# Performance work log

Hardware: AMD Instinct MI355X
Metric: run time of the kernel (lower is better)

Reference implementation:

```python
import jax, jax.numpy as jnp
import numpy as np

N, M, E = 400000, 100000, 3200000
C_FEAT = 61            # per-point feature channels
D_IN = 64              # 3 (rel xyz) + C_FEAT
D0, D1, D2 = 64, 128, 256  # mlp = [64, 128, 256]
EPS = 1e-5


def setup_inputs() -> dict:
    key = jax.random.key(0)
    ks = jax.random.split(key, 16)
    inp = {}
    inp['point_bxyz'] = jax.random.uniform(ks[0], (N, 4), dtype=jnp.float32) * 50.0
    inp['point_feat'] = jax.random.normal(ks[1], (N, C_FEAT), dtype=jnp.float32)
    inp['sample_idx'] = jax.random.randint(ks[2], (M,), 0, N)
    inp['e_point'] = jax.random.randint(ks[3], (E,), 0, N)
    inp['e_new'] = jnp.sort(jax.random.randint(ks[4], (E,), 0, M))
    # PointConv: Linear(D_IN -> D0)
    inp['W0'] = jax.random.normal(ks[5], (D_IN, D0), dtype=jnp.float32) / np.sqrt(D_IN)
    inp['b0'] = jnp.zeros((D0,), dtype=jnp.float32)
    # mlp_convs[0]: Linear(D0 -> D1) + BN
    inp['W1'] = jax.random.normal(ks[6], (D0, D1), dtype=jnp.float32) / np.sqrt(D0)
    inp['b1'] = jnp.zeros((D1,), dtype=jnp.float32)
    inp['g1'] = jnp.ones((D1,), dtype=jnp.float32)
    inp['beta1'] = jnp.zeros((D1,), dtype=jnp.float32)
    # mlp_convs[1]: Linear(D1 -> D2) + BN
    inp['W2'] = jax.random.normal(ks[7], (D1, D2), dtype=jnp.float32) / np.sqrt(D1)
    inp['b2'] = jnp.zeros((D2,), dtype=jnp.float32)
    inp['g2'] = jnp.ones((D2,), dtype=jnp.float32)
    inp['beta2'] = jnp.zeros((D2,), dtype=jnp.float32)
    return inp


def _bn_relu(x, g, b):
    # BatchNorm1d in training mode: batch stats, biased variance
    mu = x.mean(axis=0)
    var = x.var(axis=0)
    return jax.nn.relu((x - mu) * jax.lax.rsqrt(var + EPS) * g + b)


def reference(point_bxyz, point_feat, sample_idx, e_point, e_new,
              W0, b0, W1, b1, g1, beta1, W2, b2, g2, beta2):
    num_new = sample_idx.shape[0]
    new_bxyz = point_bxyz[sample_idx]                      # [M, 4]
    # PointConv: per-edge relative position encoding + feature gather
    rel = point_bxyz[e_point, 1:4] - new_bxyz[e_new, 1:4]  # [E, 3]
    edge_in = jnp.concatenate([rel, point_feat[e_point]], axis=-1)  # [E, D_IN]
    h = jax.nn.relu(edge_in @ W0 + b0)                     # [E, D0]
    # per-neighborhood max aggregation (scatter-max), empty segments -> 0
    agg = jax.ops.segment_max(h, e_new, num_segments=num_new)
    agg = jnp.where(jnp.isneginf(agg), 0.0, agg)           # [M, D0]
    # trailing Linear + BN + ReLU stack
    x = _bn_relu(agg @ W1 + b1, g1, beta1)                 # [M, D1]
    x = _bn_relu(x @ W2 + b2, g2, beta2)                   # [M, D2]
    return new_bxyz, x
```

## Files before the change

kernel.cpp:

```cpp
#include <hip/hip_runtime.h>

#define EPS 1e-5f
#define ECHUNK 64

typedef _Float16 half8 __attribute__((ext_vector_type(8)));
typedef _Float16 half4v __attribute__((ext_vector_type(4)));
typedef float float4v __attribute__((ext_vector_type(4)));

static __device__ __forceinline__ unsigned pkmax16(unsigned a, unsigned b) {
    unsigned d;
    asm("v_pk_max_f16 %0, %1, %2" : "=v"(d) : "v"(a), "v"(b));
    return d;
}

__global__ void gather_kernel(const float4* __restrict__ bxyz, const int* __restrict__ sidx,
                              float4* __restrict__ out, int M) {
    int i = blockIdx.x * blockDim.x + threadIdx.x;
    if (i < M) out[i] = bxyz[sidx[i]];
}

__global__ void prep_kernel(const float* __restrict__ W0, const float* __restrict__ W1,
                            const float* __restrict__ W2, _Float16* __restrict__ W0t,
                            _Float16* __restrict__ W1t, _Float16* __restrict__ W2t) {
    int i = blockIdx.x * blockDim.x + threadIdx.x;
    if (i < 4096) {
        int k = i >> 6, n = i & 63;
        W0t[(size_t)n * 64 + k] = (_Float16)W0[i];
    } else if (i < 12288) {
        int j = i - 4096; int k = j >> 7, n = j & 127;
        W1t[(size_t)n * 64 + k] = (_Float16)W1[j];
    } else if (i < 45056) {
        int j = i - 12288; int k = j >> 8, n = j & 255;
        W2t[(size_t)n * 128 + k] = (_Float16)W2[j];
    }
}

__global__ __launch_bounds__(256, 4) void point_kernel(
    const float* __restrict__ feat, const float4* __restrict__ bxyz4,
    const _Float16* __restrict__ W0t, const float* __restrict__ b0,
    _Float16* __restrict__ GDh, int N) {
    __shared__ _Float16 As[128 * 72];
    int t = threadIdx.x;
    int row0 = blockIdx.x * 128;
    if (t < 128) {
        int r = min(row0 + t, N - 1);
        float4 P = bxyz4[r];
        As[t * 72 + 0] = (_Float16)P.y;
        As[t * 72 + 1] = (_Float16)P.z;
        As[t * 72 + 2] = (_Float16)P.w;
    }
    const float* fbase = feat + (size_t)row0 * 61;
    int avail = (int)min((size_t)7808, (size_t)(N - row0) * 61);
#pragma unroll
    for (int j = 0; j < 8; ++j) {
        int base = (t + j * 256) * 4;
        if (base < avail) {
            float4 v = *(const float4*)&fbase[base];
            float fv[4] = {v.x, v.y, v.z, v.w};
#pragma unroll
            for (int u = 0; u < 4; ++u) {
                int flat = base + u;
                int r = flat / 61;
                int k = flat - r * 61;
                As[r * 72 + 3 + k] = (_Float16)fv[u];
            }
        }
    }
    __syncthreads();
    int w = t >> 6, lane = t & 63, quad = lane >> 4, l16 = lane & 15;
    int mwave = w * 32;
    float4v acc[2][4] = {};
#pragma unroll
    for (int kc = 0; kc < 2; ++kc) {
        int koff = kc * 32 + quad * 8;
        half8 af[2], bf[4];
#pragma unroll
        for (int mt = 0; mt < 2; ++mt)
            af[mt] = *(const half8*)&As[(mwave + mt * 16 + l16) * 72 + koff];
#pragma unroll
        for (int nt = 0; nt < 4; ++nt)
            bf[nt] = *(const half8*)&W0t[(size_t)(nt * 16 + l16) * 64 + koff];
#pragma unroll
        for (int mt = 0; mt < 2; ++mt)
#pragma unroll
            for (int nt = 0; nt < 4; ++nt)
                acc[mt][nt] = __builtin_amdgcn_mfma_f32_16x16x32_f16(af[mt], bf[nt], acc[mt][nt], 0, 0, 0);
    }
    float b0v[4];
#pragma unroll
    for (int nt = 0; nt < 4; ++nt) b0v[nt] = b0[nt * 16 + l16];
    __syncthreads();
#pragma unroll
    for (int mt = 0; mt < 2; ++mt)
#pragma unroll
        for (int i = 0; i < 4; ++i) {
            int rloc = mwave + mt * 16 + quad * 4 + i;
#pragma unroll
            for (int nt = 0; nt < 4; ++nt)
                As[rloc * 72 + nt * 16 + l16] = (_Float16)(acc[mt][nt][i] + b0v[nt]);
        }
    __syncthreads();
#pragma unroll
    for (int j = 0; j < 4; ++j) {
        int i8 = t + j * 256;
        int r = i8 >> 3, c8 = i8 & 7;
        if (row0 + r < N)
            *(half8*)&GDh[(size_t)(row0 + r) * 64 + c8 * 8] = *(const half8*)&As[r * 72 + c8 * 8];
    }
}

__global__ __launch_bounds__(256, 8) void edge_kernel(
    const float4* __restrict__ nbxyz4,
    const int* __restrict__ e_point, const int* __restrict__ e_new,
    const _Float16* __restrict__ GDh, const float* __restrict__ W0,
    float* __restrict__ agg, int E) {
    int lane = threadIdx.x & 63;
    int gwave = blockIdx.x * 4 + (threadIdx.x >> 6);
    int base = __builtin_amdgcn_readfirstlane(gwave * ECHUNK);
    if (base >= E) return;
    int n = min(ECHUNK, E - base);

    if (n == ECHUNK) {
        bool hi = lane >= 32;
        int c0 = lane & 31;
        int ch = c0 * 2 + (hi ? 1 : 0);
        float wx = W0[ch], wy = W0[64 + ch], wz = W0[128 + ch];
        const unsigned NEGP = 0xFBFFFBFFu;

        int ep = e_point[base + lane];
        int en = e_new[base + lane];

        int prev = __shfl_up(en, 1);
        unsigned long long bm = __ballot(lane == 0 || en != prev);
        unsigned blo = __builtin_amdgcn_readfirstlane((unsigned)bm);
        unsigned bhi = __builtin_amdgcn_readfirstlane((unsigned)(bm >> 32));
        unsigned long long bmask = (((unsigned long long)bhi << 32) | blo) & ~1ull;

        int curseg = __builtin_amdgcn_readlane(en, 0);
        unsigned amax = NEGP;
        int laneoff = c0 * 4;
        int permbase = hi ? 4 : 0;

#define FLUSH_SEG()  do {                                                          \
        unsigned other_ = (unsigned)__shfl_xor((int)amax, 32);                     \
        unsigned comb_ = pkmax16(amax, other_);                                    \
        unsigned bits_ = hi ? (comb_ >> 16) : (comb_ & 0xffffu);                   \
        _Float16 hm_ = __builtin_bit_cast(_Float16, (unsigned short)bits_);        \
        float4 Q_ = nbxyz4[curseg];                                                \
        float S_ = fmaf(Q_.y, wx, fmaf(Q_.z, wy, Q_.w * wz));                      \
        float v_ = fmaxf(0.f, (float)hm_ - S_);                                    \
        atomicMax((int*)&agg[(size_t)curseg * 64 + ch], __float_as_int(v_));       \
    } while (0)

#pragma unroll
        for (int grp = 0; grp < 2; ++grp) {
            unsigned gu[16];
#pragma unroll
            for (int j = 0; j < 16; ++j) {
                int p = __builtin_amdgcn_ds_bpermute(permbase + (grp * 16 + j) * 8, ep);
                unsigned off = ((unsigned)p << 7) + laneoff;
                gu[j] = *(const unsigned*)((const char*)GDh + off);
            }
#pragma unroll
            for (int j = 0; j < 16; ++j) {
                int e0 = (grp * 16 + j) * 2;
                if ((bmask >> e0) & 1) {
                    FLUSH_SEG();
                    curseg = __builtin_amdgcn_readlane(en, e0);
                    amax = NEGP;
                }
                if ((bmask >> (e0 + 1)) & 1) {
                    amax = pkmax16(amax, hi ? NEGP : gu[j]);
                    FLUSH_SEG();
                    curseg = __builtin_amdgcn_readlane(en, e0 + 1);
                    amax = hi ? gu[j] : NEGP;
                } else {
                    amax = pkmax16(amax, gu[j]);
                }
            }
        }
        FLUSH_SEG();
#undef FLUSH_SEG
    } else {
        float wx = W0[lane], wy = W0[64 + lane], wz = W0[128 + lane];
        int idx = min(base + lane, E - 1);
        int ep = e_point[idx];
        int en = e_new[idx];
        int curseg = -1;
        float runmax = 0.f, S = 0.f;
        for (int e = 0; e < n; ++e) {
            int p = __builtin_amdgcn_readlane(ep, e);
            int s = __builtin_amdgcn_readlane(en, e);
            if (s != curseg) {
                if (curseg >= 0)
                    atomicMax((int*)&agg[(size_t)curseg * 64 + lane], __float_as_int(runmax));
                curseg = s;
                runmax = 0.f;
                float4 Q = nbxyz4[s];
                S = fmaf(Q.y, wx, fmaf(Q.z, wy, Q.w * wz));
            }
            float h = (float)GDh[(size_t)p * 64 + lane] - S;
            runmax = fmaxf(runmax, h);
        }
        if (curseg >= 0)
            atomicMax((int*)&agg[(size_t)curseg * 64 + lane], __float_as_int(runmax));
    }
}

__global__ __launch_bounds__(256, 2) void gemm1_kernel(
    const float* __restrict__ agg, const _Float16* __restrict__ W1t,
    _Float16* __restrict__ y1h, float* __restrict__ p1sum, float* __restrict__ p1sq, int M) {
    __shared__ _Float16 As[128 * 72];
    __shared__ float red[4096];
    int t = threadIdx.x;
    int row0 = blockIdx.x * 128;
#pragma unroll
    for (int j = 0; j < 8; ++j) {
        int i4 = t + j * 256;
        int r = i4 >> 4, k4 = i4 & 15;
        float4 v = make_float4(0.f, 0.f, 0.f, 0.f);
        if (row0 + r < M) v = ((const float4*)agg)[(size_t)(row0 + r) * 16 + k4];
        half4v h;
        h[0] = (_Float16)v.x; h[1] = (_Float16)v.y; h[2] = (_Float16)v.z; h[3] = (_Float16)v.w;
        *(half4v*)&As[r * 72 + k4 * 4] = h;
    }
    __syncthreads();
    int w = t >> 6, lane = t & 63, quad = lane >> 4, l16 = lane & 15;
    int mwave = w * 32;
    float4v acc[2][8] = {};
#pragma unroll
    for (int kc = 0; kc < 2; ++kc) {
        int koff = kc * 32 + quad * 8;
        half8 af[2], bf[8];
#pragma unroll
        for (int mt = 0; mt < 2; ++mt)
            af[mt] = *(const half8*)&As[(mwave + mt * 16 + l16) * 72 + koff];
#pragma unroll
        for (int nt = 0; nt < 8; ++nt)
            bf[nt] = *(const half8*)&W1t[(size_t)(nt * 16 + l16) * 64 + koff];
#pragma unroll
        for (int mt = 0; mt < 2; ++mt)
#pragma unroll
            for (int nt = 0; nt < 8; ++nt)
                acc[mt][nt] = __builtin_amdgcn_mfma_f32_16x16x32_f16(af[mt], bf[nt], acc[mt][nt], 0, 0, 0);
    }
    float s[8] = {}, q[8] = {};
#pragma unroll
    for (int mt = 0; mt < 2; ++mt)
#pragma unroll
        for (int i = 0; i < 4; ++i)
#pragma unroll
            for (int nt = 0; nt < 8; ++nt) {
                float a = acc[mt][nt][i];
                s[nt] += a; q[nt] += a * a;
            }
    int slot = w * 4 + quad;
#pragma unroll
    for (int nt = 0; nt < 8; ++nt) {
        int c = nt * 16 + l16;
        red[c * 16 + slot] = s[nt];
        red[2048 + c * 16 + slot] = q[nt];
    }
    __syncthreads();
    if (t < 128) {
        float ss = 0.f, qq = 0.f;
#pragma unroll
        for (int i = 0; i < 16; ++i) { ss += red[t * 16 + i]; qq += red[2048 + t * 16 + i]; }
        p1sum[(size_t)blockIdx.x * 128 + t] = ss;
        p1sq[(size_t)blockIdx.x * 128 + t] = qq;
    }
#pragma unroll
    for (int half = 0; half < 2; ++half) {
#pragma unroll
        for (int mt = 0; mt < 2; ++mt)
#pragma unroll
            for (int i = 0; i < 4; ++i) {
                int rloc = mwave + mt * 16 + quad * 4 + i;
#pragma unroll
                for (int nt = 0; nt < 4; ++nt)
                    As[rloc * 72 + nt * 16 + l16] = (_Float16)acc[mt][half * 4 + nt][i];
            }
        __syncthreads();
#pragma unroll
        for (int j = 0; j < 4; ++j) {
            int i8 = t + j * 256;
            int r = i8 >> 3, c8 = i8 & 7;
            if (row0 + r < M)
                *(half8*)&y1h[(size_t)(row0 + r) * 128 + half * 64 + c8 * 8] =
                    *(const half8*)&As[r * 72 + c8 * 8];
        }
        __syncthreads();
    }
}

__global__ void stats_kernel(const float* __restrict__ psum, const float* __restrict__ psq,
                             const float* __restrict__ g, const float* __restrict__ beta,
                             float* __restrict__ scale, float* __restrict__ shift,
                             int nblk, int ncols, float invM) {
    __shared__ float ss[256], qq[256];
    int c = blockIdx.x;
    int t = threadIdx.x;
    float s = 0.f, q = 0.f;
    for (int b = t; b < nblk; b += 256) {
        s += psum[(size_t)b * ncols + c];
        q += psq[(size_t)b * ncols + c];
    }
    ss[t] = s; qq[t] = q;
    __syncthreads();
    for (int off = 128; off > 0; off >>= 1) {
        if (t < off) { ss[t] += ss[t + off]; qq[t] += qq[t + off]; }
        __syncthreads();
    }
    if (t == 0) {
        float mean = ss[0] * invM;
        float var = qq[0] * invM - mean * mean;
        float sc = g[c] * rsqrtf(var + EPS);
        scale[c] = sc;
        shift[c] = beta[c] - mean * sc;
    }
}

__global__ __launch_bounds__(256, 2) void gemm2_kernel(
    const _Float16* __restrict__ y1h, const _Float16* __restrict__ W2t,
    const float* __restrict__ scale1, const float* __restrict__ shift1,
    float* __restrict__ yout, float* __restrict__ p2sum, float* __restrict__ p2sq,
    int M, int nbn) {
    __shared__ _Float16 As[128 * 136];
    __shared__ _Float16 Bs[128 * 136];
    int t = threadIdx.x;
    int bm = blockIdx.x / nbn;
    int bn = blockIdx.x % nbn;
    int row0 = bm * 128;
#pragma unroll
    for (int j = 0; j < 8; ++j) {
        int i8 = t + j * 256;
        int r = i8 >> 4, k8 = i8 & 15;
        half8 hv = {};
        if (row0 + r < M) {
            half8 y = *(const half8*)&y1h[(size_t)(row0 + r) * 128 + k8 * 8];
            float4 sca = ((const float4*)scale1)[k8 * 2];
            float4 scb = ((const float4*)scale1)[k8 * 2 + 1];
            float4 sha = ((const float4*)shift1)[k8 * 2];
            float4 shb = ((const float4*)shift1)[k8 * 2 + 1];
            float sc[8] = {sca.x, sca.y, sca.z, sca.w, scb.x, scb.y, scb.z, scb.w};
            float sh[8] = {sha.x, sha.y, sha.z, sha.w, shb.x, shb.y, shb.z, shb.w};
#pragma unroll
            for (int u = 0; u < 8; ++u)
                hv[u] = (_Float16)fmaxf(0.f, fmaf((float)y[u], sc[u], sh[u]));
        }
        *(half8*)&As[r * 136 + k8 * 8] = hv;
    }
    int n0 = bn * 128;
#pragma unroll
    for (int j = 0; j < 8; ++j) {
        int i8 = t + j * 256;
        int nn = i8 >> 4, k8 = i8 & 15;
        *(half8*)&Bs[nn * 136 + k8 * 8] = *(const half8*)&W2t[(size_t)(n0 + nn) * 128 + k8 * 8];
    }
    __syncthreads();
    int w = t >> 6, lane = t & 63;
    int quad = lane >> 4, l16 = lane & 15;
    int mwave = (w >> 1) * 64, nwave = (w & 1) * 64;
    float4v acc[4][4] = {};
#pragma unroll
    for (int kc = 0; kc < 4; ++kc) {
        int koff = kc * 32 + quad * 8;
        half8 af[4], bf[4];
#pragma unroll
        for (int mt = 0; mt < 4; ++mt)
            af[mt] = *(const half8*)&As[(mwave + mt * 16 + l16) * 136 + koff];
#pragma unroll
        for (int nt = 0; nt < 4; ++nt)
            bf[nt] = *(const half8*)&Bs[(nwave + nt * 16 + l16) * 136 + koff];
#pragma unroll
        for (int mt = 0; mt < 4; ++mt)
#pragma unroll
            for (int nt = 0; nt < 4; ++nt)
                acc[mt][nt] = __builtin_amdgcn_mfma_f32_16x16x32_f16(af[mt], bf[nt], acc[mt][nt], 0, 0, 0);
    }
    float s[4] = {}, q[4] = {};
    int colbase = n0 + nwave + l16;
#pragma unroll
    for (int mt = 0; mt < 4; ++mt) {
#pragma unroll
        for (int i = 0; i < 4; ++i) {
            int row = row0 + mwave + mt * 16 + quad * 4 + i;
            if (row < M) {
#pragma unroll
                for (int nt = 0; nt < 4; ++nt)
                    yout[(size_t)row * 256 + colbase + nt * 16] = acc[mt][nt][i];
            }
#pragma unroll
            for (int nt = 0; nt < 4; ++nt) {
                float a = acc[mt][nt][i];
                s[nt] += a; q[nt] += a * a;
            }
        }
    }
    __syncthreads();
    float* red = (float*)As;
    int slot = (w >> 1) * 4 + quad;
#pragma unroll
    for (int nt = 0; nt < 4; ++nt) {
        int c = (w & 1) * 64 + nt * 16 + l16;
        red[c * 8 + slot] = s[nt];
        red[1024 + c * 8 + slot] = q[nt];
    }
    __syncthreads();
    if (t < 128) {
        float ss = 0.f, qq = 0.f;
#pragma unroll
        for (int i = 0; i < 8; ++i) { ss += red[t * 8 + i]; qq += red[1024 + t * 8 + i]; }
        p2sum[(size_t)bm * 256 + n0 + t] = ss;
        p2sq[(size_t)bm * 256 + n0 + t] = qq;
    }
}

__global__ void apply2_kernel(float4* __restrict__ x, const float* __restrict__ scale2,
                              const float* __restrict__ shift2, int n4) {
    int i = blockIdx.x * blockDim.x + threadIdx.x;
    if (i >= n4) return;
    int c4 = i & 63;
    float4 v = x[i];
    float4 sc = ((const float4*)scale2)[c4];
    float4 sh = ((const float4*)shift2)[c4];
    v.x = fmaxf(0.f, fmaf(v.x, sc.x, sh.x));
    v.y = fmaxf(0.f, fmaf(v.y, sc.y, sh.y));
    v.z = fmaxf(0.f, fmaf(v.z, sc.z, sh.z));
    v.w = fmaxf(0.f, fmaf(v.w, sc.w, sh.w));
    x[i] = v;
}

extern "C" void kernel_launch(void* const* d_in, const int* in_sizes, int n_in,
                              void* d_out, int out_size, void* d_ws, size_t ws_size,
                              hipStream_t stream) {
    const float* bxyz  = (const float*)d_in[0];
    const float* feat  = (const float*)d_in[1];
    const int*   sidx  = (const int*)d_in[2];
    const int*   e_point = (const int*)d_in[3];
    const int*   e_new = (const int*)d_in[4];
    const float* W0    = (const float*)d_in[5];
    const float* b0    = (const float*)d_in[6];
    const float* W1    = (const float*)d_in[7];
    const float* g1    = (const float*)d_in[9];
    const float* beta1 = (const float*)d_in[10];
    const float* W2    = (const float*)d_in[11];
    const float* g2    = (const float*)d_in[13];
    const float* beta2 = (const float*)d_in[14];
    int N = in_sizes[0] / 4;
    int M = in_sizes[2];
    int E = in_sizes[3];

    float* out0 = (float*)d_out;
    float* out1 = (float*)d_out + (size_t)M * 4;

    float* ws = (float*)d_ws;
    size_t o = 0;
    float* agg = ws + o; o += (size_t)M * 64;
    _Float16* y1h = (_Float16*)(ws + o); o += (size_t)M * 64;
    _Float16* GDh = (_Float16*)(ws + o); o += (size_t)N * 32;
    _Float16* W0t = (_Float16*)(ws + o); o += 2048;
    _Float16* W1t = (_Float16*)(ws + o); o += 4096;
    _Float16* W2t = (_Float16*)(ws + o); o += 16384;
    int nblk1 = (M + 127) / 128;
    int nblk2m = (M + 127) / 128;
    int nbn = 2;
    float* p1sum = ws + o; o += (size_t)nblk1 * 128;
    float* p1sq  = ws + o; o += (size_t)nblk1 * 128;
    float* p2sum = ws + o; o += (size_t)nblk2m * 256;
    float* p2sq  = ws + o; o += (size_t)nblk2m * 256;
    float* scale1 = ws + o; o += 128;
    float* shift1 = ws + o; o += 128;
    float* scale2 = ws + o; o += 256;
    float* shift2 = ws + o; o += 256;

    hipMemsetAsync(agg, 0, (size_t)M * 64 * sizeof(float), stream);
    gather_kernel<<<(M + 255) / 256, 256, 0, stream>>>((const float4*)bxyz, sidx, (float4*)out0, M);
    prep_kernel<<<176, 256, 0, stream>>>(W0, W1, W2, W0t, W1t, W2t);
    point_kernel<<<(N + 127) / 128, 256, 0, stream>>>(feat, (const float4*)bxyz, W0t, b0, GDh, N);
    int nwaves = (E + ECHUNK - 1) / ECHUNK;
    edge_kernel<<<(nwaves + 3) / 4, 256, 0, stream>>>((const float4*)out0, e_point, e_new,
                                                      GDh, W0, agg, E);
    gemm1_kernel<<<nblk1, 256, 0, stream>>>(agg, W1t, y1h, p1sum, p1sq, M);
    stats_kernel<<<128, 256, 0, stream>>>(p1sum, p1sq, g1, beta1, scale1, shift1, nblk1, 128, 1.f / M);
    gemm2_kernel<<<nblk2m * nbn, 256, 0, stream>>>(y1h, W2t, scale1, shift1, out1, p2sum, p2sq, M, nbn);
    stats_kernel<<<256, 256, 0, stream>>>(p2sum, p2sq, g2, beta2, scale2, shift2, nblk2m, 256, 1.f / M);
    apply2_kernel<<<((M * 64) + 255) / 256, 256, 0, stream>>>((float4*)out1, scale2, shift2, M * 64);
}
```

Measured before the change: 389.0 us.

## Widen edge gathers to 8 bytes, store GEMM2 output as fp16, merge prep kernels

The edge kernel now processes four edges per wave step, with each lane loading 8 bytes of the gathered fp16 row instead of 4. This halves the bpermute/load iterations, at the cost of a more complex segment-boundary flush that reduces across lanes 16 and 32. GEMM2 writes its pre-BN output as fp16 through shared memory into the reused GDh buffer instead of fp32 directly to the output, so apply2 reads half the bytes. The gather and weight-prep kernels are merged into one launch. The fp16 intermediate adds rounding error before BN.

```diff
diff --git a/kernel.cpp b/kernel.cpp
--- a/kernel.cpp
+++ b/kernel.cpp
@@ -6,22 +6,25 @@
 typedef _Float16 half8 __attribute__((ext_vector_type(8)));
 typedef _Float16 half4v __attribute__((ext_vector_type(4)));
 typedef float float4v __attribute__((ext_vector_type(4)));
+typedef unsigned uint2v __attribute__((ext_vector_type(2)));
 
 static __device__ __forceinline__ unsigned pkmax16(unsigned a, unsigned b) {
     unsigned d;
     asm("v_pk_max_f16 %0, %1, %2" : "=v"(d) : "v"(a), "v"(b));
     return d;
 }
-
-__global__ void gather_kernel(const float4* __restrict__ bxyz, const int* __restrict__ sidx,
-                              float4* __restrict__ out, int M) {
-    int i = blockIdx.x * blockDim.x + threadIdx.x;
-    if (i < M) out[i] = bxyz[sidx[i]];
-}
-
-__global__ void prep_kernel(const float* __restrict__ W0, const float* __restrict__ W1,
-                            const float* __restrict__ W2, _Float16* __restrict__ W0t,
-                            _Float16* __restrict__ W1t, _Float16* __restrict__ W2t) {
+static __device__ __forceinline__ uint2v pkmax2(uint2v a, uint2v b) {
+    uint2v d;
+    d.x = pkmax16(a.x, b.x);
+    d.y = pkmax16(a.y, b.y);
+    return d;
+}
+
+__global__ void prep_gather_kernel(const float* __restrict__ W0, const float* __restrict__ W1,
+                                   const float* __restrict__ W2, _Float16* __restrict__ W0t,
+                                   _Float16* __restrict__ W1t, _Float16* __restrict__ W2t,
+                                   const float4* __restrict__ bxyz, const int* __restrict__ sidx,
+                                   float4* __restrict__ out, int M) {
     int i = blockIdx.x * blockDim.x + threadIdx.x;
     if (i < 4096) {
         int k = i >> 6, n = i & 63;
@@ -32,6 +35,9 @@
     } else if (i < 45056) {
         int j = i - 12288; int k = j >> 8, n = j & 255;
         W2t[(size_t)n * 128 + k] = (_Float16)W2[j];
+    } else {
+        int j = i - 45056;
+        if (j < M) out[j] = bxyz[sidx[j]];
     }
 }
 
@@ -121,62 +127,71 @@
     int n = min(ECHUNK, E - base);
 
     if (n == ECHUNK) {
-        bool hi = lane >= 32;
-        int c0 = lane & 31;
-        int ch = c0 * 2 + (hi ? 1 : 0);
+        int g = lane >> 4;
+        int c0 = lane & 15;
+        int ch = c0 * 4 + g;
         float wx = W0[ch], wy = W0[64 + ch], wz = W0[128 + ch];
-        const unsigned NEGP = 0xFBFFFBFFu;
+        const uint2v NEGP2 = {0xFBFFFBFFu, 0xFBFFFBFFu};
 
         int ep = e_point[base + lane];
         int en = e_new[base + lane];
 
         int prev = __shfl_up(en, 1);
-        unsigned long long bm = __ballot(lane == 0 || en != prev);
-        unsigned blo = __builtin_amdgcn_readfirstlane((unsigned)bm);
-        unsigned bhi = __builtin_amdgcn_readfirstlane((unsigned)(bm >> 32));
+        unsigned long long bmball = __ballot(lane == 0 || en != prev);
+        unsigned blo = __builtin_amdgcn_readfirstlane((unsigned)bmball);
+        unsigned bhi = __builtin_amdgcn_readfirstlane((unsigned)(bmball >> 32));
         unsigned long long bmask = (((unsigned long long)bhi << 32) | blo) & ~1ull;
 
         int curseg = __builtin_amdgcn_readlane(en, 0);
-        unsigned amax = NEGP;
-        int laneoff = c0 * 4;
-        int permbase = hi ? 4 : 0;
-
-#define FLUSH_SEG()  do {                                                          \
-        unsigned other_ = (unsigned)__shfl_xor((int)amax, 32);                     \
-        unsigned comb_ = pkmax16(amax, other_);                                    \
-        unsigned bits_ = hi ? (comb_ >> 16) : (comb_ & 0xffffu);                   \
-        _Float16 hm_ = __builtin_bit_cast(_Float16, (unsigned short)bits_);        \
-        float4 Q_ = nbxyz4[curseg];                                                \
-        float S_ = fmaf(Q_.y, wx, fmaf(Q_.z, wy, Q_.w * wz));                      \
-        float v_ = fmaxf(0.f, (float)hm_ - S_);                                    \
-        atomicMax((int*)&agg[(size_t)curseg * 64 + ch], __float_as_int(v_));       \
+        uint2v amax = NEGP2;
+        int laneoff = c0 * 8;
+        int permbase = g * 4;
+
+#define FLUSH_SEG()  do {                                                           \
+        unsigned ax_ = pkmax16(amax.x, (unsigned)__shfl_xor((int)amax.x, 16));      \
+        ax_ = pkmax16(ax_, (unsigned)__shfl_xor((int)ax_, 32));                     \
+        unsigned ay_ = pkmax16(amax.y, (unsigned)__shfl_xor((int)amax.y, 16));      \
+        ay_ = pkmax16(ay_, (unsigned)__shfl_xor((int)ay_, 32));                     \
+        unsigned sel_ = (g & 2) ? ay_ : ax_;                                        \
+        unsigned bits_ = (g & 1) ? (sel_ >> 16) : (sel_ & 0xffffu);                 \
+        _Float16 hm_ = __builtin_bit_cast(_Float16, (unsigned short)bits_);         \
+        float4 Q_ = nbxyz4[curseg];                                                 \
+        float S_ = fmaf(Q_.y, wx, fmaf(Q_.z, wy, Q_.w * wz));                       \
+        float v_ = fmaxf(0.f, (float)hm_ - S_);                                     \
+        atomicMax((int*)&agg[(size_t)curseg * 64 + ch], __float_as_int(v_));        \
     } while (0)
 
 #pragma unroll
         for (int grp = 0; grp < 2; ++grp) {
-            unsigned gu[16];
-#pragma unroll
-            for (int j = 0; j < 16; ++j) {
-                int p = __builtin_amdgcn_ds_bpermute(permbase + (grp * 16 + j) * 8, ep);
+            uint2v gu[8];
+#pragma unroll
+            for (int j = 0; j < 8; ++j) {
+                int p = __builtin_amdgcn_ds_bpermute(permbase + (grp * 8 + j) * 16, ep);
                 unsigned off = ((unsigned)p << 7) + laneoff;
-                gu[j] = *(const unsigned*)((const char*)GDh + off);
-            }
-#pragma unroll
-            for (int j = 0; j < 16; ++j) {
-                int e0 = (grp * 16 + j) * 2;
+                gu[j] = *(const uint2v*)((const char*)GDh + off);
+            }
+#pragma unroll
+            for (int j = 0; j < 8; ++j) {
+                int e0 = (grp * 8 + j) * 4;
                 if ((bmask >> e0) & 1) {
                     FLUSH_SEG();
                     curseg = __builtin_amdgcn_readlane(en, e0);
-                    amax = NEGP;
+                    amax = NEGP2;
                 }
-                if ((bmask >> (e0 + 1)) & 1) {
-                    amax = pkmax16(amax, hi ? NEGP : gu[j]);
-                    FLUSH_SEG();
-                    curseg = __builtin_amdgcn_readlane(en, e0 + 1);
-                    amax = hi ? gu[j] : NEGP;
-                } else {
-                    amax = pkmax16(amax, gu[j]);
+                int start = 0;
+#pragma unroll
+                for (int b = 1; b < 4; ++b) {
+                    if ((bmask >> (e0 + b)) & 1) {
+                        uint2v contrib = (g >= start && g < b) ? gu[j] : NEGP2;
+                        amax = pkmax2(amax, contrib);
+                        FLUSH_SEG();
+                        curseg = __builtin_amdgcn_readlane(en, e0 + b);
+                        amax = NEGP2;
+                        start = b;
+                    }
                 }
+                uint2v tail = (g >= start) ? gu[j] : NEGP2;
+                amax = pkmax2(amax, tail);
             }
         }
         FLUSH_SEG();
@@ -323,7 +338,7 @@
 __global__ __launch_bounds__(256, 2) void gemm2_kernel(
     const _Float16* __restrict__ y1h, const _Float16* __restrict__ W2t,
     const float* __restrict__ scale1, const float* __restrict__ shift1,
-    float* __restrict__ yout, float* __restrict__ p2sum, float* __restrict__ p2sq,
+    _Float16* __restrict__ y2h, float* __restrict__ p2sum, float* __restrict__ p2sq,
     int M, int nbn) {
     __shared__ _Float16 As[128 * 136];
     __shared__ _Float16 Bs[128 * 136];
@@ -379,26 +394,17 @@
                 acc[mt][nt] = __builtin_amdgcn_mfma_f32_16x16x32_f16(af[mt], bf[nt], acc[mt][nt], 0, 0, 0);
     }
     float s[4] = {}, q[4] = {};
-    int colbase = n0 + nwave + l16;
-#pragma unroll
-    for (int mt = 0; mt < 4; ++mt) {
-#pragma unroll
-        for (int i = 0; i < 4; ++i) {
-            int row = row0 + mwave + mt * 16 + quad * 4 + i;
-            if (row < M) {
-#pragma unroll
-                for (int nt = 0; nt < 4; ++nt)
-                    yout[(size_t)row * 256 + colbase + nt * 16] = acc[mt][nt][i];
-            }
+#pragma unroll
+    for (int mt = 0; mt < 4; ++mt)
+#pragma unroll
+        for (int i = 0; i < 4; ++i)
 #pragma unroll
             for (int nt = 0; nt < 4; ++nt) {
                 float a = acc[mt][nt][i];
                 s[nt] += a; q[nt] += a * a;
             }
-        }
-    }
-    __syncthreads();
-    float* red = (float*)As;
+    __syncthreads();
+    float* red = (float*)Bs;
     int slot = (w >> 1) * 4 + quad;
 #pragma unroll
     for (int nt = 0; nt < 4; ++nt) {
@@ -406,6 +412,15 @@
         red[c * 8 + slot] = s[nt];
         red[1024 + c * 8 + slot] = q[nt];
     }
+#pragma unroll
+    for (int mt = 0; mt < 4; ++mt)
+#pragma unroll
+        for (int i = 0; i < 4; ++i) {
+            int rloc = mwave + mt * 16 + quad * 4 + i;
+#pragma unroll
+            for (int nt = 0; nt < 4; ++nt)
+                As[rloc * 136 + nwave + nt * 16 + l16] = (_Float16)acc[mt][nt][i];
+        }
     __syncthreads();
     if (t < 128) {
         float ss = 0.f, qq = 0.f;
@@ -414,21 +429,38 @@
         p2sum[(size_t)bm * 256 + n0 + t] = ss;
         p2sq[(size_t)bm * 256 + n0 + t] = qq;
     }
-}
-
-__global__ void apply2_kernel(float4* __restrict__ x, const float* __restrict__ scale2,
-                              const float* __restrict__ shift2, int n4) {
+#pragma unroll
+    for (int j = 0; j < 8; ++j) {
+        int i8 = t + j * 256;
+        int r = i8 >> 4, c8 = i8 & 15;
+        if (row0 + r < M)
+            *(half8*)&y2h[(size_t)(row0 + r) * 256 + n0 + c8 * 8] =
+                *(const half8*)&As[r * 136 + c8 * 8];
+    }
+}
+
+__global__ void apply2_kernel(const _Float16* __restrict__ y2h, float4* __restrict__ x,
+                              const float* __restrict__ scale2, const float* __restrict__ shift2,
+                              int n8) {
     int i = blockIdx.x * blockDim.x + threadIdx.x;
-    if (i >= n4) return;
-    int c4 = i & 63;
-    float4 v = x[i];
-    float4 sc = ((const float4*)scale2)[c4];
-    float4 sh = ((const float4*)shift2)[c4];
-    v.x = fmaxf(0.f, fmaf(v.x, sc.x, sh.x));
-    v.y = fmaxf(0.f, fmaf(v.y, sc.y, sh.y));
-    v.z = fmaxf(0.f, fmaf(v.z, sc.z, sh.z));
-    v.w = fmaxf(0.f, fmaf(v.w, sc.w, sh.w));
-    x[i] = v;
+    if (i >= n8) return;
+    int c8 = i & 31;
+    half8 y = *(const half8*)&y2h[(size_t)i * 8];
+    float4 sc0 = ((const float4*)scale2)[c8 * 2];
+    float4 sc1 = ((const float4*)scale2)[c8 * 2 + 1];
+    float4 sh0 = ((const float4*)shift2)[c8 * 2];
+    float4 sh1 = ((const float4*)shift2)[c8 * 2 + 1];
+    float4 a, b;
+    a.x = fmaxf(0.f, fmaf((float)y[0], sc0.x, sh0.x));
+    a.y = fmaxf(0.f, fmaf((float)y[1], sc0.y, sh0.y));
+    a.z = fmaxf(0.f, fmaf((float)y[2], sc0.z, sh0.z));
+    a.w = fmaxf(0.f, fmaf((float)y[3], sc0.w, sh0.w));
+    b.x = fmaxf(0.f, fmaf((float)y[4], sc1.x, sh1.x));
+    b.y = fmaxf(0.f, fmaf((float)y[5], sc1.y, sh1.y));
+    b.z = fmaxf(0.f, fmaf((float)y[6], sc1.z, sh1.z));
+    b.w = fmaxf(0.f, fmaf((float)y[7], sc1.w, sh1.w));
+    x[(size_t)i * 2] = a;
+    x[(size_t)i * 2 + 1] = b;
 }
 
 extern "C" void kernel_launch(void* const* d_in, const int* in_sizes, int n_in,
@@ -473,17 +505,19 @@
     float* shift1 = ws + o; o += 128;
     float* scale2 = ws + o; o += 256;
     float* shift2 = ws + o; o += 256;
+    _Float16* y2h = GDh;
 
     hipMemsetAsync(agg, 0, (size_t)M * 64 * sizeof(float), stream);
-    gather_kernel<<<(M + 255) / 256, 256, 0, stream>>>((const float4*)bxyz, sidx, (float4*)out0, M);
-    prep_kernel<<<176, 256, 0, stream>>>(W0, W1, W2, W0t, W1t, W2t);
+    int ngpg = (45056 + M + 255) / 256;
+    prep_gather_kernel<<<ngpg, 256, 0, stream>>>(W0, W1, W2, W0t, W1t, W2t,
+                                                 (const float4*)bxyz, sidx, (float4*)out0, M);
     point_kernel<<<(N + 127) / 128, 256, 0, stream>>>(feat, (const float4*)bxyz, W0t, b0, GDh, N);
     int nwaves = (E + ECHUNK - 1) / ECHUNK;
     edge_kernel<<<(nwaves + 3) / 4, 256, 0, stream>>>((const float4*)out0, e_point, e_new,
                                                       GDh, W0, agg, E);
     gemm1_kernel<<<nblk1, 256, 0, stream>>>(agg, W1t, y1h, p1sum, p1sq, M);
     stats_kernel<<<128, 256, 0, stream>>>(p1sum, p1sq, g1, beta1, scale1, shift1, nblk1, 128, 1.f / M);
-    gemm2_kernel<<<nblk2m * nbn, 256, 0, stream>>>(y1h, W2t, scale1, shift1, out1, p2sum, p2sq, M, nbn);
+    gemm2_kernel<<<nblk2m * nbn, 256, 0, stream>>>(y1h, W2t, scale1, shift1, y2h, p2sum, p2sq, M, nbn);
     stats_kernel<<<256, 256, 0, stream>>>(p2sum, p2sq, g2, beta2, scale2, shift2, nblk2m, 256, 1.f / M);
-    apply2_kernel<<<((M * 64) + 255) / 256, 256, 0, stream>>>((float4*)out1, scale2, shift2, M * 64);
-}
+    apply2_kernel<<<((M * 32) + 255) / 256, 256, 0, stream>>>(y2h, (float4*)out1, scale2, shift2, M * 32);
+}
```

New measurement: 384.6 us. Within noise of the previous version (-1.1%).
